# Optimization experiments

Measured on AMD Instinct MI355X. Metric: run time of the kernel, lower is better.

The kernel has to match this reference:

```python
import jax, jax.numpy as jnp
import numpy as np

HIDDEN = 1024
INTER = 4096
EPS = 1e-12


def _ste(q, x):
    # straight-through estimator: forward q, backward identity wrt x
    return x + jax.lax.stop_gradient(q - x)


def setup_inputs() -> dict:
    key = jax.random.key(0)
    ks = jax.random.split(key, 4)
    hidden_states = jax.random.normal(ks[0], (4, 2048, INTER), dtype=jnp.float32)
    input_tensor = jax.random.normal(ks[1], (4, 2048, HIDDEN), dtype=jnp.float32)
    W = jax.random.normal(ks[2], (HIDDEN, INTER), dtype=jnp.float32) * 0.02
    b = jnp.zeros((HIDDEN,), dtype=jnp.float32)
    clip_val = jnp.asarray(2.5, dtype=jnp.float32)  # learnable elastic alpha
    gamma = jnp.ones((HIDDEN,), dtype=jnp.float32)
    beta = jnp.zeros((HIDDEN,), dtype=jnp.float32)
    return {"hidden_states": hidden_states, "input_tensor": input_tensor,
            "W": W, "b": b, "clip_val": clip_val, "gamma": gamma, "beta": beta}


def reference(hidden_states, input_tensor, W, b, clip_val, gamma, beta):
    # --- binary weight (BWN): per-output-channel scale = mean(|W|, axis=in) ---
    w_scale = jnp.mean(jnp.abs(W), axis=1, keepdims=True)  # [hidden, 1]
    W_q = _ste(w_scale * jnp.sign(W), W)                    # [hidden, inter]
    # --- elastic signed binary activation: q = alpha * sign(x / alpha) ---
    s = hidden_states / clip_val
    x_q = clip_val * _ste(jnp.sign(s), s)                   # [b, s, inter]
    # --- dense projection ---
    h = jnp.einsum('bsi,hi->bsh', x_q, W_q) + b             # [b, s, hidden]
    # dropout prob 0.0 (eval mode) -> no-op
    # --- residual + LayerNorm (eps=1e-12) ---
    r = h + input_tensor
    mu = jnp.mean(r, axis=-1, keepdims=True)
    var = jnp.mean(jnp.square(r - mu), axis=-1, keepdims=True)
    out = (r - mu) * jax.lax.rsqrt(var + EPS) * gamma + beta
    return out
```

## Files before the change

### kernel.cpp

```cpp
#include <hip/hip_runtime.h>
#include <stdint.h>

#define HIDDEN 1024
#define INTER  4096
#define ROWS   8192
#define BM     32
#define BK     64
#define NKSTEP 64
#define NBLK   256
#define BTILE  65536

typedef int i32x4 __attribute__((ext_vector_type(4)));
typedef const uint32_t __attribute__((address_space(1))) gu32;
typedef uint32_t __attribute__((address_space(3))) lu32;

__device__ __forceinline__ uint32_t sgn4(float4 v) {
    uint32_t b0 = (v.x < 0.f) ? 0xFFu : 0x01u;
    uint32_t b1 = (v.y < 0.f) ? 0xFFu : 0x01u;
    uint32_t b2 = (v.z < 0.f) ? 0xFFu : 0x01u;
    uint32_t b3 = (v.w < 0.f) ? 0xFFu : 0x01u;
    return b0 | (b1 << 8) | (b2 << 16) | (b3 << 24);
}

__global__ __launch_bounds__(256)
void pack_w_kernel(const float* __restrict__ W, uint8_t* __restrict__ Bg,
                   float* __restrict__ wscale) {
    int h = blockIdx.x;
    int tid = threadIdx.x;
    int lane = tid & 63, wv = tid >> 6;
    const float4* row = (const float4*)(W + (size_t)h * INTER);
    const uint32_t base_h = (uint32_t)(h >> 4) * 1024u + (uint32_t)(h & 15) * 16u;
    float asum = 0.f;
    #pragma unroll
    for (int q = 0; q < 4; ++q) {
        int g = q * 256 + tid;
        float4 v = row[g];
        asum += fabsf(v.x) + fabsf(v.y) + fabsf(v.z) + fabsf(v.w);
        uint32_t off = (uint32_t)(g >> 4) * (uint32_t)BTILE + base_h
                     + (uint32_t)((g & 15) >> 2) * 256u + (uint32_t)(g & 3) * 4u;
        *(uint32_t*)(Bg + off) = sgn4(v);
    }
    #pragma unroll
    for (int off = 32; off > 0; off >>= 1) asum += __shfl_down(asum, off);
    __shared__ float red[4];
    if (lane == 0) red[wv] = asum;
    __syncthreads();
    if (tid == 0) wscale[h] = (red[0] + red[1] + red[2] + red[3]) * (1.0f / INTER);
}

__global__ __launch_bounds__(512, 2)
void main_kernel(const float* __restrict__ hs, const uint8_t* __restrict__ Bg,
                 const float* __restrict__ wscale, const float* __restrict__ bias,
                 const float* __restrict__ clipp, const float* __restrict__ input,
                 const float* __restrict__ gamma, const float* __restrict__ beta,
                 float* __restrict__ out) {
    __shared__ alignas(16) uint8_t sB[2 * BTILE];
    __shared__ alignas(16) uint8_t sA[2 * 2048];
    __shared__ float s_mu[BM], s_rs[BM];

    const int tid  = threadIdx.x;
    const int lane = tid & 63;
    const int wave = tid >> 6;
    const int m0   = blockIdx.x * BM;

    const int ar = tid >> 4;
    const int ac = tid & 15;
    const int awofs = (ar >> 4) * 1024 + ((ac >> 2) * 16 + (ar & 15)) * 16 + (ac & 3) * 4;
    const float* aload = hs + (size_t)(m0 + ar) * INTER + ac * 4;

    const uint8_t* bsrc = Bg + wave * 8192 + lane * 16;
    uint8_t* bdst0 = sB + wave * 8192;
    const int fofs = lane * 16;

    i32x4 acc0[8], acc1[8];
    #pragma unroll
    for (int ct = 0; ct < 8; ++ct) {
        acc0[ct] = (i32x4){0, 0, 0, 0};
        acc1[ct] = (i32x4){0, 0, 0, 0};
    }

    float4 av0 = *(const float4*)(aload);
    #pragma unroll
    for (int j = 0; j < 8; ++j)
        __builtin_amdgcn_global_load_lds((gu32*)(bsrc + j * 1024),
                                         (lu32*)(bdst0 + j * 1024), 16, 0, 0);
    float4 av1 = *(const float4*)(aload + 64);
    #pragma unroll
    for (int j = 0; j < 8; ++j)
        __builtin_amdgcn_global_load_lds((gu32*)(bsrc + BTILE + j * 1024),
                                         (lu32*)(bdst0 + BTILE + j * 1024), 16, 0, 0);
    *(uint32_t*)&sA[awofs] = sgn4(av0);
    asm volatile("s_waitcnt lgkmcnt(0)" ::: "memory");
    __builtin_amdgcn_s_barrier();

#define GEMM_BODY(T, CUR, DO_WRITE, DO_ISSUE, VM, AVW, AVL) do {              \
    asm volatile("s_waitcnt vmcnt(" #VM ")" ::: "memory");                    \
    const uint8_t* bb_ = sB + (CUR) * BTILE + wave * 8192;                    \
    i32x4 a0_ = *(const i32x4*)&sA[(CUR) * 2048 + fofs];                      \
    i32x4 a1_ = *(const i32x4*)&sA[(CUR) * 2048 + 1024 + fofs];               \
    _Pragma("unroll")                                                         \
    for (int ct_ = 0; ct_ < 8; ++ct_) {                                       \
        i32x4 bf_ = *(const i32x4*)&bb_[ct_ * 1024 + fofs];                   \
        acc0[ct_] = __builtin_amdgcn_mfma_i32_16x16x64_i8(a0_, bf_, acc0[ct_], 0, 0, 0); \
        acc1[ct_] = __builtin_amdgcn_mfma_i32_16x16x64_i8(a1_, bf_, acc1[ct_], 0, 0, 0); \
    }                                                                         \
    if (DO_WRITE) *(uint32_t*)&sA[((CUR) ^ 1) * 2048 + awofs] = sgn4(AVW);    \
    asm volatile("s_waitcnt lgkmcnt(0)" ::: "memory");                        \
    if (DO_ISSUE) {                                                           \
        AVL = *(const float4*)(aload + ((T) + 2) * 64);                       \
        _Pragma("unroll")                                                     \
        for (int j_ = 0; j_ < 8; ++j_)                                        \
            __builtin_amdgcn_global_load_lds(                                 \
                (gu32*)(bsrc + (size_t)((T) + 2) * BTILE + j_ * 1024),        \
                (lu32*)(bdst0 + (CUR) * BTILE + j_ * 1024), 16, 0, 0);        \
    }                                                                         \
    __builtin_amdgcn_s_barrier();                                             \
} while (0)

    for (int tt = 0; tt < 31; ++tt) {
        const int t0 = 2 * tt;
        GEMM_BODY(t0,     0, 1, 1, 9, av1, av0);
        GEMM_BODY(t0 + 1, 1, 1, 1, 9, av0, av1);
    }
    GEMM_BODY(62, 0, 1, 0, 9, av1, av0);
    GEMM_BODY(63, 1, 0, 0, 0, av0, av0);
#undef GEMM_BODY

    float clip = clipp[0];
    const int l15 = lane & 15;
    const int hb  = wave * 128 + l15;
    const int rb  = (lane >> 4) * 4;
    float cw[8], bi[8];
    #pragma unroll
    for (int ct = 0; ct < 8; ++ct) {
        cw[ct] = clip * wscale[hb + ct * 16];
        bi[ct] = bias[hb + ct * 16];
    }

    float* yl = (float*)sB;
    #pragma unroll
    for (int ct = 0; ct < 8; ++ct) {
        #pragma unroll
        for (int rg = 0; rg < 4; ++rg) {
            yl[(rb + rg) * HIDDEN + hb + ct * 16]      = fmaf((float)acc0[ct][rg], cw[ct], bi[ct]);
            yl[(16 + rb + rg) * HIDDEN + hb + ct * 16] = fmaf((float)acc1[ct][rg], cw[ct], bi[ct]);
        }
    }
    __syncthreads();

    const int erow = tid >> 4;
    const int ecol = tid & 15;
    const float4* in4 = (const float4*)(input + (size_t)(m0 + erow) * HIDDEN);
    float4* ylr = (float4*)(yl + erow * HIDDEN);
    float s = 0.f, q = 0.f;
    #pragma unroll
    for (int i = 0; i < 16; ++i) {
        int f = ecol + i * 16;
        float4 y4 = ylr[f];
        float4 r4 = in4[f];
        y4.x += r4.x; y4.y += r4.y; y4.z += r4.z; y4.w += r4.w;
        s += y4.x + y4.y + y4.z + y4.w;
        q += y4.x * y4.x + y4.y * y4.y + y4.z * y4.z + y4.w * y4.w;
        ylr[f] = y4;
    }
    #pragma unroll
    for (int off = 1; off <= 8; off <<= 1) {
        s += __shfl_xor(s, off);
        q += __shfl_xor(q, off);
    }
    if (ecol == 0) {
        float mu  = s * (1.0f / HIDDEN);
        float var = fmaf(-mu, mu, q * (1.0f / HIDDEN));
        s_mu[erow] = mu;
        s_rs[erow] = rsqrtf(var + 1e-12f);
    }
    __syncthreads();

    const float4* gm4 = (const float4*)gamma;
    const float4* bt4 = (const float4*)beta;
    const float4* yv  = (const float4*)yl;
    float4* outp = (float4*)(out + (size_t)m0 * HIDDEN);
    #pragma unroll
    for (int j = 0; j < 16; ++j) {
        int f  = j * 512 + tid;
        int rl = f >> 8;
        int c4 = f & 255;
        float4 y4 = yv[f];
        float4 g4 = gm4[c4], b4 = bt4[c4];
        float mu = s_mu[rl], rs = s_rs[rl];
        float4 o;
        o.x = (y4.x - mu) * rs * g4.x + b4.x;
        o.y = (y4.y - mu) * rs * g4.y + b4.y;
        o.z = (y4.z - mu) * rs * g4.z + b4.z;
        o.w = (y4.w - mu) * rs * g4.w + b4.w;
        outp[f] = o;
    }
}

extern "C" void kernel_launch(void* const* d_in, const int* in_sizes, int n_in,
                              void* d_out, int out_size, void* d_ws, size_t ws_size,
                              hipStream_t stream) {
    const float* hs    = (const float*)d_in[0];
    const float* inp   = (const float*)d_in[1];
    const float* W     = (const float*)d_in[2];
    const float* b     = (const float*)d_in[3];
    const float* clip  = (const float*)d_in[4];
    const float* gamma = (const float*)d_in[5];
    const float* beta  = (const float*)d_in[6];
    float* out = (float*)d_out;

    uint8_t* Bg   = (uint8_t*)d_ws;
    float* wscale = (float*)((char*)d_ws + (size_t)NKSTEP * BTILE);

    pack_w_kernel<<<HIDDEN, 256, 0, stream>>>(W, Bg, wscale);
    main_kernel<<<NBLK, 512, 0, stream>>>(hs, Bg, wscale, b, clip,
                                          inp, gamma, beta, out);
}
```

Baseline: 295.4 us.

## Fuse weight packing into cooperative GEMM kernel with 64x512 tiles and split LayerNorm

Merges the weight-binarization kernel and the main GEMM+LayerNorm kernel into one cooperative launch that uses grid.sync between phases. The GEMM tile moves from 32 rows by all 1024 columns to 64 rows by 512 columns, so each activation row is packed by two blocks and B traffic per MFMA drops. LayerNorm statistics are reduced across the two column halves through a workspace and a second grid sync. The aim is to remove a kernel launch and improve the MFMA-to-load ratio. In exchange it adds two grid-wide barriers and relies on all 256 blocks being co-resident.

```diff
diff --git a/kernel.cpp b/kernel.cpp
--- a/kernel.cpp
+++ b/kernel.cpp
@@ -1,13 +1,17 @@
 #include <hip/hip_runtime.h>
+#include <hip/hip_cooperative_groups.h>
 #include <stdint.h>
+
+namespace cg = cooperative_groups;
 
 #define HIDDEN 1024
 #define INTER  4096
 #define ROWS   8192
-#define BM     32
+#define NBLK   256
+#define BM     64
+#define BN     512
 #define BK     64
 #define NKSTEP 64
-#define NBLK   256
 #define BTILE  65536
 
 typedef int i32x4 __attribute__((ext_vector_type(4)));
@@ -22,178 +26,213 @@
     return b0 | (b1 << 8) | (b2 << 16) | (b3 << 24);
 }
 
-__global__ __launch_bounds__(256)
-void pack_w_kernel(const float* __restrict__ W, uint8_t* __restrict__ Bg,
-                   float* __restrict__ wscale) {
-    int h = blockIdx.x;
-    int tid = threadIdx.x;
-    int lane = tid & 63, wv = tid >> 6;
-    const float4* row = (const float4*)(W + (size_t)h * INTER);
-    const uint32_t base_h = (uint32_t)(h >> 4) * 1024u + (uint32_t)(h & 15) * 16u;
-    float asum = 0.f;
-    #pragma unroll
-    for (int q = 0; q < 4; ++q) {
-        int g = q * 256 + tid;
-        float4 v = row[g];
-        asum += fabsf(v.x) + fabsf(v.y) + fabsf(v.z) + fabsf(v.w);
-        uint32_t off = (uint32_t)(g >> 4) * (uint32_t)BTILE + base_h
-                     + (uint32_t)((g & 15) >> 2) * 256u + (uint32_t)(g & 3) * 4u;
-        *(uint32_t*)(Bg + off) = sgn4(v);
-    }
-    #pragma unroll
-    for (int off = 32; off > 0; off >>= 1) asum += __shfl_down(asum, off);
-    __shared__ float red[4];
-    if (lane == 0) red[wv] = asum;
-    __syncthreads();
-    if (tid == 0) wscale[h] = (red[0] + red[1] + red[2] + red[3]) * (1.0f / INTER);
-}
-
 __global__ __launch_bounds__(512, 2)
-void main_kernel(const float* __restrict__ hs, const uint8_t* __restrict__ Bg,
-                 const float* __restrict__ wscale, const float* __restrict__ bias,
-                 const float* __restrict__ clipp, const float* __restrict__ input,
-                 const float* __restrict__ gamma, const float* __restrict__ beta,
-                 float* __restrict__ out) {
-    __shared__ alignas(16) uint8_t sB[2 * BTILE];
-    __shared__ alignas(16) uint8_t sA[2 * 2048];
-    __shared__ float s_mu[BM], s_rs[BM];
+void fused_kernel(const float* __restrict__ hs, const float* __restrict__ input,
+                  const float* __restrict__ W, const float* __restrict__ bias,
+                  const float* __restrict__ clipp, const float* __restrict__ gamma,
+                  const float* __restrict__ beta, float* __restrict__ out,
+                  uint8_t* __restrict__ Bg, float* __restrict__ wscale,
+                  float2* __restrict__ sqws) {
+    __shared__ alignas(16) uint8_t smem[131072 + 1024];
+    uint8_t* sB   = smem;
+    uint8_t* sA   = smem + 65536;
+    float*   s_mu = (float*)(smem + 131072);
+    float*   s_rs = (float*)(smem + 131072 + 256);
+    float*   redp = (float*)(smem + 131072 + 512);
 
     const int tid  = threadIdx.x;
     const int lane = tid & 63;
     const int wave = tid >> 6;
-    const int m0   = blockIdx.x * BM;
-
-    const int ar = tid >> 4;
-    const int ac = tid & 15;
-    const int awofs = (ar >> 4) * 1024 + ((ac >> 2) * 16 + (ar & 15)) * 16 + (ac & 3) * 4;
-    const float* aload = hs + (size_t)(m0 + ar) * INTER + ac * 4;
-
-    const uint8_t* bsrc = Bg + wave * 8192 + lane * 16;
-    uint8_t* bdst0 = sB + wave * 8192;
+    cg::grid_group grid = cg::this_grid();
+
+    {
+        const int h   = blockIdx.x * 4 + (tid >> 7);
+        const int pos = tid & 127;
+        const float4* row = (const float4*)(W + (size_t)h * INTER);
+        const uint32_t base_h = (uint32_t)(h >> 4) * 1024u + (uint32_t)(h & 15) * 16u;
+        float asum = 0.f;
+        #pragma unroll
+        for (int j = 0; j < 8; ++j) {
+            int g = pos + j * 128;
+            float4 v = row[g];
+            asum += fabsf(v.x) + fabsf(v.y) + fabsf(v.z) + fabsf(v.w);
+            uint32_t off = (uint32_t)(g >> 4) * (uint32_t)BTILE + base_h
+                         + (uint32_t)((g & 15) >> 2) * 256u + (uint32_t)(g & 3) * 4u;
+            *(uint32_t*)(Bg + off) = sgn4(v);
+        }
+        #pragma unroll
+        for (int off = 32; off > 0; off >>= 1) asum += __shfl_down(asum, off);
+        if (lane == 0) redp[wave] = asum;
+        __syncthreads();
+        if (tid < 4)
+            wscale[blockIdx.x * 4 + tid] = (redp[2 * tid] + redp[2 * tid + 1]) * (1.0f / INTER);
+    }
+    grid.sync();
+
+    const int m0 = (blockIdx.x >> 1) * BM;
+    const int ch = blockIdx.x & 1;
+
+    const int r  = tid >> 3;
+    const int c8 = tid & 7;
+    const int awofs = (r >> 4) * 1024 + ((c8 >> 1) * 16 + (r & 15)) * 16 + (c8 & 1) * 8;
+    const float4* aload = (const float4*)(hs + (size_t)(m0 + r) * INTER + c8 * 8);
+
+    const uint8_t* bsrc = Bg + (ch * 32 + wave * 4) * 1024 + lane * 16;
+    uint8_t* bdst = sB + wave * 4096;
     const int fofs = lane * 16;
 
-    i32x4 acc0[8], acc1[8];
-    #pragma unroll
-    for (int ct = 0; ct < 8; ++ct) {
-        acc0[ct] = (i32x4){0, 0, 0, 0};
-        acc1[ct] = (i32x4){0, 0, 0, 0};
-    }
-
-    float4 av0 = *(const float4*)(aload);
-    #pragma unroll
-    for (int j = 0; j < 8; ++j)
+    i32x4 acc[4][4];
+    #pragma unroll
+    for (int rt = 0; rt < 4; ++rt)
+        #pragma unroll
+        for (int cf = 0; cf < 4; ++cf) acc[rt][cf] = (i32x4){0, 0, 0, 0};
+
+    float4 avA0 = aload[0], avA1 = aload[1];
+    #pragma unroll
+    for (int j = 0; j < 4; ++j)
         __builtin_amdgcn_global_load_lds((gu32*)(bsrc + j * 1024),
-                                         (lu32*)(bdst0 + j * 1024), 16, 0, 0);
-    float4 av1 = *(const float4*)(aload + 64);
-    #pragma unroll
-    for (int j = 0; j < 8; ++j)
+                                         (lu32*)(bdst + j * 1024), 16, 0, 0);
+    float4 avB0 = aload[16], avB1 = aload[17];
+    #pragma unroll
+    for (int j = 0; j < 4; ++j)
         __builtin_amdgcn_global_load_lds((gu32*)(bsrc + BTILE + j * 1024),
-                                         (lu32*)(bdst0 + BTILE + j * 1024), 16, 0, 0);
-    *(uint32_t*)&sA[awofs] = sgn4(av0);
+                                         (lu32*)(bdst + 32768 + j * 1024), 16, 0, 0);
+    *(uint32_t*)&sA[awofs]     = sgn4(avA0);
+    *(uint32_t*)&sA[awofs + 4] = sgn4(avA1);
     asm volatile("s_waitcnt lgkmcnt(0)" ::: "memory");
     __builtin_amdgcn_s_barrier();
 
-#define GEMM_BODY(T, CUR, DO_WRITE, DO_ISSUE, VM, AVW, AVL) do {              \
+#define GEMM_BODY(T, CUR, DO_WRITE, DO_ISSUE, VM, AW0, AW1, AL0, AL1) do {    \
     asm volatile("s_waitcnt vmcnt(" #VM ")" ::: "memory");                    \
-    const uint8_t* bb_ = sB + (CUR) * BTILE + wave * 8192;                    \
-    i32x4 a0_ = *(const i32x4*)&sA[(CUR) * 2048 + fofs];                      \
-    i32x4 a1_ = *(const i32x4*)&sA[(CUR) * 2048 + 1024 + fofs];               \
+    const uint8_t* bb_ = sB + (CUR) * 32768 + wave * 4096;                    \
+    const uint8_t* ab_ = sA + (CUR) * 4096;                                   \
+    i32x4 af0_ = *(const i32x4*)&ab_[fofs];                                   \
+    i32x4 af1_ = *(const i32x4*)&ab_[1024 + fofs];                            \
+    i32x4 af2_ = *(const i32x4*)&ab_[2048 + fofs];                            \
+    i32x4 af3_ = *(const i32x4*)&ab_[3072 + fofs];                            \
     _Pragma("unroll")                                                         \
-    for (int ct_ = 0; ct_ < 8; ++ct_) {                                       \
-        i32x4 bf_ = *(const i32x4*)&bb_[ct_ * 1024 + fofs];                   \
-        acc0[ct_] = __builtin_amdgcn_mfma_i32_16x16x64_i8(a0_, bf_, acc0[ct_], 0, 0, 0); \
-        acc1[ct_] = __builtin_amdgcn_mfma_i32_16x16x64_i8(a1_, bf_, acc1[ct_], 0, 0, 0); \
+    for (int cf_ = 0; cf_ < 4; ++cf_) {                                       \
+        i32x4 bf_ = *(const i32x4*)&bb_[cf_ * 1024 + fofs];                   \
+        acc[0][cf_] = __builtin_amdgcn_mfma_i32_16x16x64_i8(af0_, bf_, acc[0][cf_], 0, 0, 0); \
+        acc[1][cf_] = __builtin_amdgcn_mfma_i32_16x16x64_i8(af1_, bf_, acc[1][cf_], 0, 0, 0); \
+        acc[2][cf_] = __builtin_amdgcn_mfma_i32_16x16x64_i8(af2_, bf_, acc[2][cf_], 0, 0, 0); \
+        acc[3][cf_] = __builtin_amdgcn_mfma_i32_16x16x64_i8(af3_, bf_, acc[3][cf_], 0, 0, 0); \
     }                                                                         \
-    if (DO_WRITE) *(uint32_t*)&sA[((CUR) ^ 1) * 2048 + awofs] = sgn4(AVW);    \
+    if (DO_WRITE) {                                                           \
+        *(uint32_t*)&sA[((CUR) ^ 1) * 4096 + awofs]     = sgn4(AW0);          \
+        *(uint32_t*)&sA[((CUR) ^ 1) * 4096 + awofs + 4] = sgn4(AW1);          \
+    }                                                                         \
     asm volatile("s_waitcnt lgkmcnt(0)" ::: "memory");                        \
     if (DO_ISSUE) {                                                           \
-        AVL = *(const float4*)(aload + ((T) + 2) * 64);                       \
+        AL0 = aload[((T) + 2) * 16];                                          \
+        AL1 = aload[((T) + 2) * 16 + 1];                                      \
         _Pragma("unroll")                                                     \
-        for (int j_ = 0; j_ < 8; ++j_)                                        \
+        for (int j_ = 0; j_ < 4; ++j_)                                        \
             __builtin_amdgcn_global_load_lds(                                 \
                 (gu32*)(bsrc + (size_t)((T) + 2) * BTILE + j_ * 1024),        \
-                (lu32*)(bdst0 + (CUR) * BTILE + j_ * 1024), 16, 0, 0);        \
+                (lu32*)(bdst + (CUR) * 32768 + j_ * 1024), 16, 0, 0);         \
     }                                                                         \
     __builtin_amdgcn_s_barrier();                                             \
 } while (0)
 
     for (int tt = 0; tt < 31; ++tt) {
         const int t0 = 2 * tt;
-        GEMM_BODY(t0,     0, 1, 1, 9, av1, av0);
-        GEMM_BODY(t0 + 1, 1, 1, 1, 9, av0, av1);
-    }
-    GEMM_BODY(62, 0, 1, 0, 9, av1, av0);
-    GEMM_BODY(63, 1, 0, 0, 0, av0, av0);
+        GEMM_BODY(t0,     0, 1, 1, 6, avB0, avB1, avA0, avA1);
+        GEMM_BODY(t0 + 1, 1, 1, 1, 6, avA0, avA1, avB0, avB1);
+    }
+    GEMM_BODY(62, 0, 1, 0, 6, avB0, avB1, avA0, avA1);
+    GEMM_BODY(63, 1, 0, 0, 0, avA0, avA1, avB0, avB1);
 #undef GEMM_BODY
 
-    float clip = clipp[0];
+    __syncthreads();
+
+    const float clip = clipp[0];
     const int l15 = lane & 15;
-    const int hb  = wave * 128 + l15;
-    const int rb  = (lane >> 4) * 4;
-    float cw[8], bi[8];
-    #pragma unroll
-    for (int ct = 0; ct < 8; ++ct) {
-        cw[ct] = clip * wscale[hb + ct * 16];
-        bi[ct] = bias[hb + ct * 16];
-    }
-
-    float* yl = (float*)sB;
-    #pragma unroll
-    for (int ct = 0; ct < 8; ++ct) {
-        #pragma unroll
-        for (int rg = 0; rg < 4; ++rg) {
-            yl[(rb + rg) * HIDDEN + hb + ct * 16]      = fmaf((float)acc0[ct][rg], cw[ct], bi[ct]);
-            yl[(16 + rb + rg) * HIDDEN + hb + ct * 16] = fmaf((float)acc1[ct][rg], cw[ct], bi[ct]);
+    const int rq  = (lane >> 4) * 4;
+    float cw[4], bi[4];
+    #pragma unroll
+    for (int cf = 0; cf < 4; ++cf) {
+        int gcol = ch * BN + wave * 64 + cf * 16 + l15;
+        cw[cf] = clip * wscale[gcol];
+        bi[cf] = bias[gcol];
+    }
+
+    float* yl = (float*)smem;
+    #pragma unroll
+    for (int rt = 0; rt < 4; ++rt)
+        #pragma unroll
+        for (int cf = 0; cf < 4; ++cf)
+            #pragma unroll
+            for (int rg = 0; rg < 4; ++rg) {
+                int rw = rt * 16 + rq + rg;
+                int cl = wave * 64 + cf * 16 + l15;
+                yl[rw * BN + cl] = fmaf((float)acc[rt][cf][rg], cw[cf], bi[cf]);
+            }
+    __syncthreads();
+
+    float4* yl4 = (float4*)yl;
+    const float4* in4 = (const float4*)input;
+    float s8[8], q8[8];
+    #pragma unroll
+    for (int j = 0; j < 8; ++j) { s8[j] = 0.f; q8[j] = 0.f; }
+    #pragma unroll
+    for (int j = 0; j < 16; ++j) {
+        int g   = wave * 16 + j;
+        int idx = g * 64 + lane;
+        int rw  = idx >> 7;
+        float4 y4 = yl4[idx];
+        float4 r4 = in4[(size_t)(m0 + rw) * 256 + ch * 128 + (idx & 127)];
+        y4.x += r4.x; y4.y += r4.y; y4.z += r4.z; y4.w += r4.w;
+        yl4[idx] = y4;
+        s8[j >> 1] += y4.x + y4.y + y4.z + y4.w;
+        q8[j >> 1] += y4.x * y4.x + y4.y * y4.y + y4.z * y4.z + y4.w * y4.w;
+    }
+    #pragma unroll
+    for (int off = 1; off < 64; off <<= 1)
+        #pragma unroll
+        for (int j = 0; j < 8; ++j) {
+            s8[j] += __shfl_xor(s8[j], off);
+            q8[j] += __shfl_xor(q8[j], off);
         }
-    }
-    __syncthreads();
-
-    const int erow = tid >> 4;
-    const int ecol = tid & 15;
-    const float4* in4 = (const float4*)(input + (size_t)(m0 + erow) * HIDDEN);
-    float4* ylr = (float4*)(yl + erow * HIDDEN);
-    float s = 0.f, q = 0.f;
-    #pragma unroll
-    for (int i = 0; i < 16; ++i) {
-        int f = ecol + i * 16;
-        float4 y4 = ylr[f];
-        float4 r4 = in4[f];
-        y4.x += r4.x; y4.y += r4.y; y4.z += r4.z; y4.w += r4.w;
-        s += y4.x + y4.y + y4.z + y4.w;
-        q += y4.x * y4.x + y4.y * y4.y + y4.z * y4.z + y4.w * y4.w;
-        ylr[f] = y4;
-    }
-    #pragma unroll
-    for (int off = 1; off <= 8; off <<= 1) {
-        s += __shfl_xor(s, off);
-        q += __shfl_xor(q, off);
-    }
-    if (ecol == 0) {
+    if (lane == 0) {
+        #pragma unroll
+        for (int j = 0; j < 8; ++j)
+            sqws[(size_t)(m0 + wave * 8 + j) * 2 + ch] = make_float2(s8[j], q8[j]);
+    }
+
+    grid.sync();
+
+    if (tid < BM) {
+        float2 p0 = sqws[(size_t)(m0 + tid) * 2 + 0];
+        float2 p1 = sqws[(size_t)(m0 + tid) * 2 + 1];
+        float s = p0.x + p1.x, q = p0.y + p1.y;
         float mu  = s * (1.0f / HIDDEN);
         float var = fmaf(-mu, mu, q * (1.0f / HIDDEN));
-        s_mu[erow] = mu;
-        s_rs[erow] = rsqrtf(var + 1e-12f);
+        s_mu[tid] = mu;
+        s_rs[tid] = rsqrtf(var + 1e-12f);
     }
     __syncthreads();
 
     const float4* gm4 = (const float4*)gamma;
     const float4* bt4 = (const float4*)beta;
-    const float4* yv  = (const float4*)yl;
-    float4* outp = (float4*)(out + (size_t)m0 * HIDDEN);
+    float4 g0 = gm4[ch * 128 + lane], g1 = gm4[ch * 128 + 64 + lane];
+    float4 b0 = bt4[ch * 128 + lane], b1 = bt4[ch * 128 + 64 + lane];
+    float4* out4 = (float4*)out;
     #pragma unroll
     for (int j = 0; j < 16; ++j) {
-        int f  = j * 512 + tid;
-        int rl = f >> 8;
-        int c4 = f & 255;
-        float4 y4 = yv[f];
-        float4 g4 = gm4[c4], b4 = bt4[c4];
-        float mu = s_mu[rl], rs = s_rs[rl];
+        int g   = wave * 16 + j;
+        int idx = g * 64 + lane;
+        int rw  = idx >> 7;
+        float4 y4 = yl4[idx];
+        float4 gg = (j & 1) ? g1 : g0;
+        float4 bb = (j & 1) ? b1 : b0;
+        float mu = s_mu[rw], rs = s_rs[rw];
         float4 o;
-        o.x = (y4.x - mu) * rs * g4.x + b4.x;
-        o.y = (y4.y - mu) * rs * g4.y + b4.y;
-        o.z = (y4.z - mu) * rs * g4.z + b4.z;
-        o.w = (y4.w - mu) * rs * g4.w + b4.w;
-        outp[f] = o;
+        o.x = (y4.x - mu) * rs * gg.x + bb.x;
+        o.y = (y4.y - mu) * rs * gg.y + bb.y;
+        o.z = (y4.z - mu) * rs * gg.z + bb.z;
+        o.w = (y4.w - mu) * rs * gg.w + bb.w;
+        out4[(size_t)(m0 + rw) * 256 + ch * 128 + (idx & 127)] = o;
     }
 }
 
@@ -210,9 +249,12 @@
     float* out = (float*)d_out;
 
     uint8_t* Bg   = (uint8_t*)d_ws;
-    float* wscale = (float*)((char*)d_ws + (size_t)NKSTEP * BTILE);
-
-    pack_w_kernel<<<HIDDEN, 256, 0, stream>>>(W, Bg, wscale);
-    main_kernel<<<NBLK, 512, 0, stream>>>(hs, Bg, wscale, b, clip,
-                                          inp, gamma, beta, out);
+    float* wscale = (float*)((char*)d_ws + 4u * 1024u * 1024u);
+    float2* sqws  = (float2*)((char*)d_ws + 4u * 1024u * 1024u + 4096u);
+
+    void* args[] = { (void*)&hs, (void*)&inp, (void*)&W, (void*)&b, (void*)&clip,
+                     (void*)&gamma, (void*)&beta, (void*)&out,
+                     (void*)&Bg, (void*)&wscale, (void*)&sqws };
+    hipLaunchCooperativeKernel((const void*)fused_kernel, dim3(NBLK), dim3(512),
+                               args, 0, stream);
 }
```

New measurement: 379.4 us. 28.4% more time.

## Split hidden dim across two blocks, load B to registers, separate LayerNorm kernel

Applied to the files above, without the earlier changes.

The GEMM grid is doubled so each block computes a 32x512 output half instead of 32x1024. B fragments now go straight from global memory into registers instead of through LDS via global_load_lds, and MFMA issue priority is raised. Each block writes the partial residual sums to global memory, and a new ln_kernel finishes the LayerNorm. This aims for higher occupancy and more parallelism, at the cost of reading the A tile twice, an extra round trip of the output through global memory, and one more kernel launch.

```diff
diff --git a/kernel.cpp b/kernel.cpp
--- a/kernel.cpp
+++ b/kernel.cpp
@@ -5,14 +5,12 @@
 #define INTER  4096
 #define ROWS   8192
 #define BM     32
-#define BK     64
+#define BN     512
 #define NKSTEP 64
-#define NBLK   256
-#define BTILE  65536
+#define NBLK   512
+#define BSTEP  65536
 
 typedef int i32x4 __attribute__((ext_vector_type(4)));
-typedef const uint32_t __attribute__((address_space(1))) gu32;
-typedef uint32_t __attribute__((address_space(3))) lu32;
 
 __device__ __forceinline__ uint32_t sgn4(float4 v) {
     uint32_t b0 = (v.x < 0.f) ? 0xFFu : 0x01u;
@@ -36,7 +34,7 @@
         int g = q * 256 + tid;
         float4 v = row[g];
         asum += fabsf(v.x) + fabsf(v.y) + fabsf(v.z) + fabsf(v.w);
-        uint32_t off = (uint32_t)(g >> 4) * (uint32_t)BTILE + base_h
+        uint32_t off = (uint32_t)(g >> 4) * (uint32_t)BSTEP + base_h
                      + (uint32_t)((g & 15) >> 2) * 256u + (uint32_t)(g & 3) * 4u;
         *(uint32_t*)(Bg + off) = sgn4(v);
     }
@@ -48,152 +46,148 @@
     if (tid == 0) wscale[h] = (red[0] + red[1] + red[2] + red[3]) * (1.0f / INTER);
 }
 
-__global__ __launch_bounds__(512, 2)
-void main_kernel(const float* __restrict__ hs, const uint8_t* __restrict__ Bg,
-                 const float* __restrict__ wscale, const float* __restrict__ bias,
-                 const float* __restrict__ clipp, const float* __restrict__ input,
-                 const float* __restrict__ gamma, const float* __restrict__ beta,
-                 float* __restrict__ out) {
-    __shared__ alignas(16) uint8_t sB[2 * BTILE];
+__global__ __launch_bounds__(512, 4)
+void gemm_kernel(const float* __restrict__ hs, const float* __restrict__ input,
+                 const float* __restrict__ bias, const float* __restrict__ clipp,
+                 float* __restrict__ out, const uint8_t* __restrict__ Bg,
+                 const float* __restrict__ wscale, float2* __restrict__ sqws) {
+    __shared__ alignas(16) uint8_t yls[65536];
     __shared__ alignas(16) uint8_t sA[2 * 2048];
-    __shared__ float s_mu[BM], s_rs[BM];
 
     const int tid  = threadIdx.x;
     const int lane = tid & 63;
     const int wave = tid >> 6;
-    const int m0   = blockIdx.x * BM;
-
-    const int ar = tid >> 4;
-    const int ac = tid & 15;
-    const int awofs = (ar >> 4) * 1024 + ((ac >> 2) * 16 + (ar & 15)) * 16 + (ac & 3) * 4;
-    const float* aload = hs + (size_t)(m0 + ar) * INTER + ac * 4;
-
-    const uint8_t* bsrc = Bg + wave * 8192 + lane * 16;
-    uint8_t* bdst0 = sB + wave * 8192;
+    const int mt   = blockIdx.x & 255;
+    const int ch   = blockIdx.x >> 8;
+    const int m0   = mt * BM;
+
+    const int r  = tid >> 4;
+    const int c4 = tid & 15;
+    const int awofs = (r >> 4) * 1024 + ((c4 >> 2) * 16 + (r & 15)) * 16 + (c4 & 3) * 4;
+    const float* aload = hs + (size_t)(m0 + r) * INTER + c4 * 4;
+
+    const uint8_t* bbase = Bg + (size_t)(ch * 32 + wave * 4) * 1024 + lane * 16;
     const int fofs = lane * 16;
 
-    i32x4 acc0[8], acc1[8];
-    #pragma unroll
-    for (int ct = 0; ct < 8; ++ct) {
-        acc0[ct] = (i32x4){0, 0, 0, 0};
-        acc1[ct] = (i32x4){0, 0, 0, 0};
-    }
-
-    float4 av0 = *(const float4*)(aload);
-    #pragma unroll
-    for (int j = 0; j < 8; ++j)
-        __builtin_amdgcn_global_load_lds((gu32*)(bsrc + j * 1024),
-                                         (lu32*)(bdst0 + j * 1024), 16, 0, 0);
-    float4 av1 = *(const float4*)(aload + 64);
-    #pragma unroll
-    for (int j = 0; j < 8; ++j)
-        __builtin_amdgcn_global_load_lds((gu32*)(bsrc + BTILE + j * 1024),
-                                         (lu32*)(bdst0 + BTILE + j * 1024), 16, 0, 0);
-    *(uint32_t*)&sA[awofs] = sgn4(av0);
+    i32x4 acc[2][4];
+    #pragma unroll
+    for (int rt = 0; rt < 2; ++rt)
+        #pragma unroll
+        for (int cf = 0; cf < 4; ++cf) acc[rt][cf] = (i32x4){0, 0, 0, 0};
+    i32x4 Bb0[4], Bb1[4];
+
+    float4 avA = *(const float4*)aload;
+    #pragma unroll
+    for (int cf = 0; cf < 4; ++cf) Bb0[cf] = *(const i32x4*)(bbase + cf * 1024);
+    *(uint32_t*)&sA[awofs] = sgn4(avA);
+    avA = *(const float4*)(aload + 64);
     asm volatile("s_waitcnt lgkmcnt(0)" ::: "memory");
     __builtin_amdgcn_s_barrier();
 
-#define GEMM_BODY(T, CUR, DO_WRITE, DO_ISSUE, VM, AVW, AVL) do {              \
-    asm volatile("s_waitcnt vmcnt(" #VM ")" ::: "memory");                    \
-    const uint8_t* bb_ = sB + (CUR) * BTILE + wave * 8192;                    \
-    i32x4 a0_ = *(const i32x4*)&sA[(CUR) * 2048 + fofs];                      \
-    i32x4 a1_ = *(const i32x4*)&sA[(CUR) * 2048 + 1024 + fofs];               \
-    _Pragma("unroll")                                                         \
-    for (int ct_ = 0; ct_ < 8; ++ct_) {                                       \
-        i32x4 bf_ = *(const i32x4*)&bb_[ct_ * 1024 + fofs];                   \
-        acc0[ct_] = __builtin_amdgcn_mfma_i32_16x16x64_i8(a0_, bf_, acc0[ct_], 0, 0, 0); \
-        acc1[ct_] = __builtin_amdgcn_mfma_i32_16x16x64_i8(a1_, bf_, acc1[ct_], 0, 0, 0); \
-    }                                                                         \
-    if (DO_WRITE) *(uint32_t*)&sA[((CUR) ^ 1) * 2048 + awofs] = sgn4(AVW);    \
-    asm volatile("s_waitcnt lgkmcnt(0)" ::: "memory");                        \
-    if (DO_ISSUE) {                                                           \
-        AVL = *(const float4*)(aload + ((T) + 2) * 64);                       \
-        _Pragma("unroll")                                                     \
-        for (int j_ = 0; j_ < 8; ++j_)                                        \
-            __builtin_amdgcn_global_load_lds(                                 \
-                (gu32*)(bsrc + (size_t)((T) + 2) * BTILE + j_ * 1024),        \
-                (lu32*)(bdst0 + (CUR) * BTILE + j_ * 1024), 16, 0, 0);        \
-    }                                                                         \
-    __builtin_amdgcn_s_barrier();                                             \
+#define BODY(T, CUR, BC, BN_, PFB, PFA) do {                                   \
+    i32x4 af0_ = *(const i32x4*)&sA[(CUR) * 2048 + fofs];                      \
+    i32x4 af1_ = *(const i32x4*)&sA[(CUR) * 2048 + 1024 + fofs];               \
+    if (PFB) {                                                                 \
+        const uint8_t* bp_ = bbase + (size_t)((T) + 1) * BSTEP;                \
+        _Pragma("unroll")                                                      \
+        for (int cf_ = 0; cf_ < 4; ++cf_)                                      \
+            Bb##BN_[cf_] = *(const i32x4*)(bp_ + cf_ * 1024);                  \
+    }                                                                          \
+    __builtin_amdgcn_s_setprio(1);                                             \
+    _Pragma("unroll")                                                          \
+    for (int cf_ = 0; cf_ < 4; ++cf_) {                                        \
+        acc[0][cf_] = __builtin_amdgcn_mfma_i32_16x16x64_i8(af0_, Bb##BC[cf_], acc[0][cf_], 0, 0, 0); \
+        acc[1][cf_] = __builtin_amdgcn_mfma_i32_16x16x64_i8(af1_, Bb##BC[cf_], acc[1][cf_], 0, 0, 0); \
+    }                                                                          \
+    __builtin_amdgcn_s_setprio(0);                                             \
+    if (PFB) {                                                                 \
+        *(uint32_t*)&sA[((CUR) ^ 1) * 2048 + awofs] = sgn4(avA);               \
+        if (PFA) avA = *(const float4*)(aload + ((T) + 2) * 64);               \
+        asm volatile("s_waitcnt lgkmcnt(0)" ::: "memory");                     \
+        __builtin_amdgcn_s_barrier();                                          \
+    }                                                                          \
 } while (0)
 
     for (int tt = 0; tt < 31; ++tt) {
-        const int t0 = 2 * tt;
-        GEMM_BODY(t0,     0, 1, 1, 9, av1, av0);
-        GEMM_BODY(t0 + 1, 1, 1, 1, 9, av0, av1);
-    }
-    GEMM_BODY(62, 0, 1, 0, 9, av1, av0);
-    GEMM_BODY(63, 1, 0, 0, 0, av0, av0);
-#undef GEMM_BODY
-
-    float clip = clipp[0];
+        BODY(2 * tt,     0, 0, 1, 1, 1);
+        BODY(2 * tt + 1, 1, 1, 0, 1, 1);
+    }
+    BODY(62, 0, 0, 1, 1, 0);
+    BODY(63, 1, 1, 0, 0, 0);
+#undef BODY
+
+    const float clip = clipp[0];
     const int l15 = lane & 15;
-    const int hb  = wave * 128 + l15;
-    const int rb  = (lane >> 4) * 4;
-    float cw[8], bi[8];
-    #pragma unroll
-    for (int ct = 0; ct < 8; ++ct) {
-        cw[ct] = clip * wscale[hb + ct * 16];
-        bi[ct] = bias[hb + ct * 16];
-    }
-
-    float* yl = (float*)sB;
-    #pragma unroll
-    for (int ct = 0; ct < 8; ++ct) {
+    const int g4i = lane >> 4;
+    float cw[4], bi[4];
+    #pragma unroll
+    for (int cf = 0; cf < 4; ++cf) {
+        int gcol = ch * BN + wave * 64 + cf * 16 + l15;
+        cw[cf] = clip * wscale[gcol];
+        bi[cf] = bias[gcol];
+    }
+    float* yl = (float*)yls;
+    #pragma unroll
+    for (int rt = 0; rt < 2; ++rt)
         #pragma unroll
-        for (int rg = 0; rg < 4; ++rg) {
-            yl[(rb + rg) * HIDDEN + hb + ct * 16]      = fmaf((float)acc0[ct][rg], cw[ct], bi[ct]);
-            yl[(16 + rb + rg) * HIDDEN + hb + ct * 16] = fmaf((float)acc1[ct][rg], cw[ct], bi[ct]);
-        }
-    }
+        for (int cf = 0; cf < 4; ++cf)
+            #pragma unroll
+            for (int rg = 0; rg < 4; ++rg) {
+                int rw = rt * 16 + g4i * 4 + rg;
+                int cl = wave * 64 + cf * 16 + l15;
+                yl[rw * BN + cl] = fmaf((float)acc[rt][cf][rg], cw[cf], bi[cf]);
+            }
     __syncthreads();
 
-    const int erow = tid >> 4;
-    const int ecol = tid & 15;
-    const float4* in4 = (const float4*)(input + (size_t)(m0 + erow) * HIDDEN);
-    float4* ylr = (float4*)(yl + erow * HIDDEN);
+    float4* yl4 = (float4*)yl;
+    const float4* in4 = (const float4*)input;
+    float4* out4 = (float4*)out;
     float s = 0.f, q = 0.f;
     #pragma unroll
-    for (int i = 0; i < 16; ++i) {
-        int f = ecol + i * 16;
-        float4 y4 = ylr[f];
-        float4 r4 = in4[f];
+    for (int j = 0; j < 8; ++j) {
+        int idx  = r * 128 + c4 + j * 16;
+        int gidx = (int)((size_t)0) + c4 + j * 16;
+        float4 y4 = yl4[idx];
+        float4 r4 = in4[(size_t)(m0 + r) * 256 + ch * 128 + gidx];
         y4.x += r4.x; y4.y += r4.y; y4.z += r4.z; y4.w += r4.w;
+        out4[(size_t)(m0 + r) * 256 + ch * 128 + gidx] = y4;
         s += y4.x + y4.y + y4.z + y4.w;
         q += y4.x * y4.x + y4.y * y4.y + y4.z * y4.z + y4.w * y4.w;
-        ylr[f] = y4;
     }
     #pragma unroll
     for (int off = 1; off <= 8; off <<= 1) {
         s += __shfl_xor(s, off);
         q += __shfl_xor(q, off);
     }
-    if (ecol == 0) {
-        float mu  = s * (1.0f / HIDDEN);
-        float var = fmaf(-mu, mu, q * (1.0f / HIDDEN));
-        s_mu[erow] = mu;
-        s_rs[erow] = rsqrtf(var + 1e-12f);
-    }
-    __syncthreads();
-
+    if (c4 == 0) sqws[(size_t)(m0 + r) * 2 + ch] = make_float2(s, q);
+}
+
+__global__ __launch_bounds__(256)
+void ln_kernel(float* __restrict__ out, const float2* __restrict__ sqws,
+               const float* __restrict__ gamma, const float* __restrict__ beta) {
+    const int lane = threadIdx.x & 63;
+    const int wave = threadIdx.x >> 6;
+    const int row  = blockIdx.x * 4 + wave;
+    float2 p0 = sqws[(size_t)row * 2 + 0];
+    float2 p1 = sqws[(size_t)row * 2 + 1];
+    float ss = p0.x + p1.x, qq = p0.y + p1.y;
+    float mu  = ss * (1.0f / HIDDEN);
+    float var = fmaf(-mu, mu, qq * (1.0f / HIDDEN));
+    float rs  = rsqrtf(var + 1e-12f);
+    float4* rowp = (float4*)(out + (size_t)row * HIDDEN);
     const float4* gm4 = (const float4*)gamma;
     const float4* bt4 = (const float4*)beta;
-    const float4* yv  = (const float4*)yl;
-    float4* outp = (float4*)(out + (size_t)m0 * HIDDEN);
-    #pragma unroll
-    for (int j = 0; j < 16; ++j) {
-        int f  = j * 512 + tid;
-        int rl = f >> 8;
-        int c4 = f & 255;
-        float4 y4 = yv[f];
-        float4 g4 = gm4[c4], b4 = bt4[c4];
-        float mu = s_mu[rl], rs = s_rs[rl];
+    #pragma unroll
+    for (int j = 0; j < 4; ++j) {
+        int idx = lane + j * 64;
+        float4 y = rowp[idx];
+        float4 g = gm4[idx], b = bt4[idx];
         float4 o;
-        o.x = (y4.x - mu) * rs * g4.x + b4.x;
-        o.y = (y4.y - mu) * rs * g4.y + b4.y;
-        o.z = (y4.z - mu) * rs * g4.z + b4.z;
-        o.w = (y4.w - mu) * rs * g4.w + b4.w;
-        outp[f] = o;
+        o.x = (y.x - mu) * rs * g.x + b.x;
+        o.y = (y.y - mu) * rs * g.y + b.y;
+        o.z = (y.z - mu) * rs * g.z + b.z;
+        o.w = (y.w - mu) * rs * g.w + b.w;
+        rowp[idx] = o;
     }
 }
 
@@ -210,9 +204,10 @@
     float* out = (float*)d_out;
 
     uint8_t* Bg   = (uint8_t*)d_ws;
-    float* wscale = (float*)((char*)d_ws + (size_t)NKSTEP * BTILE);
+    float* wscale = (float*)((char*)d_ws + 4u * 1024u * 1024u);
+    float2* sqws  = (float2*)((char*)d_ws + 4u * 1024u * 1024u + 4096u);
 
     pack_w_kernel<<<HIDDEN, 256, 0, stream>>>(W, Bg, wscale);
-    main_kernel<<<NBLK, 512, 0, stream>>>(hs, Bg, wscale, b, clip,
-                                          inp, gamma, beta, out);
-}
+    gemm_kernel<<<NBLK, 512, 0, stream>>>(hs, inp, b, clip, out, Bg, wscale, sqws);
+    ln_kernel<<<ROWS / 4, 256, 0, stream>>>(out, sqws, gamma, beta);
+}
```

After: 298.3 us. No clear change (+1.0%).
